# Kernel tuning notes

Hardware: AMD Instinct MI355X
Metric: run time of the kernel (lower is better)

Reference implementation:

```python
import jax, jax.numpy as jnp
import numpy as np

N_NODES = 50000
N_GRAPHS = 256
IN_DIM = 128
HID = 128
N_LAYERS = 3
N_EDGES = 800000


def setup_inputs() -> dict:
    key = jax.random.key(0)
    ks = jax.random.split(key, 16)
    x = jax.random.normal(ks[0], (N_NODES, IN_DIM), dtype=jnp.float32)
    edge_index = jax.random.randint(ks[1], (2, N_EDGES), 0, N_NODES, dtype=jnp.int64)
    batch = jnp.sort(jax.random.randint(ks[2], (N_NODES,), 0, N_GRAPHS, dtype=jnp.int64))
    inp = {"x": x, "edge_index": edge_index, "batch": batch}
    # SAGEConv params per PyG: lin_l (bias) applied to mean-aggregated neighbors,
    # lin_r (no bias) applied to the root node feature.
    dims = [(IN_DIM, HID)] + [(HID, HID)] * (N_LAYERS - 1)
    for i, (din, dout) in enumerate(dims):
        s = 1.0 / np.sqrt(din)
        inp[f"Wl{i}"] = jax.random.uniform(ks[3 + 3 * i], (din, dout), jnp.float32, -s, s)
        inp[f"bl{i}"] = jax.random.uniform(ks[4 + 3 * i], (dout,), jnp.float32, -s, s)
        inp[f"Wr{i}"] = jax.random.uniform(ks[5 + 3 * i], (din, dout), jnp.float32, -s, s)
    return inp


def _sage_conv(x, src, dst, Wl, bl, Wr):
    # mean aggregation of source-node messages into destination nodes
    msg = x[src]                                               # [E, d] gather
    agg = jax.ops.segment_sum(msg, dst, num_segments=N_NODES)  # [N, d] scatter-add
    deg = jax.ops.segment_sum(jnp.ones((src.shape[0], 1), x.dtype), dst,
                              num_segments=N_NODES)
    agg = agg / jnp.maximum(deg, 1.0)
    return agg @ Wl + bl + x @ Wr


def reference(x, edge_index, batch, Wl0, bl0, Wr0, Wl1, bl1, Wr1, Wl2, bl2, Wr2):
    src, dst = edge_index[0], edge_index[1]
    params = [(Wl0, bl0, Wr0), (Wl1, bl1, Wr1), (Wl2, bl2, Wr2)]
    h = x
    for Wl, bl, Wr in params:
        h = jax.nn.relu(_sage_conv(h, src, dst, Wl, bl, Wr))
        # dropout is a no-op in eval mode
    # meanmax readout over graph ids
    cnt = jax.ops.segment_sum(jnp.ones((h.shape[0], 1), h.dtype), batch,
                              num_segments=N_GRAPHS)
    g_mean = jax.ops.segment_sum(h, batch, num_segments=N_GRAPHS) / jnp.maximum(cnt, 1.0)
    g_max = jax.ops.segment_max(h, batch, num_segments=N_GRAPHS)
    g_max = jnp.where(jnp.isfinite(g_max), g_max, 0.0)  # empty graphs -> 0
    return jnp.concatenate([g_mean, g_max], axis=-1)    # [G, 2*HID]
```

## Files before the change

### kernel.cpp

```cpp
#include <hip/hip_runtime.h>
#include <hip/hip_bf16.h>
#include <stdint.h>

#define N_NODES  50000
#define N_GRAPHS 256
#define DIM      128
#define N_EDGES  800000
#define K2       256
#define N_STRIPS (N_NODES / 16)
#define PAD_CAP  64
#define NBUCKET  196
#define NCHUNK   256
#define CHUNK    3125

typedef __attribute__((ext_vector_type(8))) short  short8;
typedef __attribute__((ext_vector_type(4))) float  floatx4;

__device__ __forceinline__ ushort f2bf(float f) {
    union { float f; uint32_t u; } c; c.f = f;
    uint32_t u = c.u;
    return (ushort)((u + 0x7fffu + ((u >> 16) & 1u)) >> 16);
}
__device__ __forceinline__ float bf2f(ushort b) {
    union { uint32_t u; float f; } c; c.u = ((uint32_t)b) << 16;
    return c.f;
}

__global__ __launch_bounds__(256) void k_convert_x(const float* __restrict__ x,
                                                   ushort* __restrict__ xb) {
    int i = blockIdx.x * 256 + threadIdx.x;
    const int n4 = N_NODES * DIM / 4;
    if (i < n4) {
        float4 v = ((const float4*)x)[i];
        uint32_t lo = (uint32_t)f2bf(v.x) | ((uint32_t)f2bf(v.y) << 16);
        uint32_t hi = (uint32_t)f2bf(v.z) | ((uint32_t)f2bf(v.w) << 16);
        ((uint2*)xb)[i] = make_uint2(lo, hi);
    }
}

__global__ __launch_bounds__(256) void k_prep_w_all(const float* __restrict__ Wl0, const float* __restrict__ Wr0,
                                                    const float* __restrict__ Wl1, const float* __restrict__ Wr1,
                                                    const float* __restrict__ Wl2, const float* __restrict__ Wr2,
                                                    ushort* __restrict__ Wt) {
    int i = blockIdx.x * 256 + threadIdx.x;
    if (i < 3 * DIM * K2) {
        int layer = i / (DIM * K2);
        int j = i % (DIM * K2);
        int n = j / K2, k = j % K2;
        const float* Wl = (layer == 0) ? Wl0 : (layer == 1) ? Wl1 : Wl2;
        const float* Wr = (layer == 0) ? Wr0 : (layer == 1) ? Wr1 : Wr2;
        float v = (k < DIM) ? Wl[k * DIM + n] : Wr[(k - DIM) * DIM + n];
        Wt[i] = f2bf(v);
    }
}

__global__ __launch_bounds__(256) void k_hist(const int* __restrict__ dst,
                                              int* __restrict__ counts) {
    __shared__ int hist[NBUCKET];
    int t = threadIdx.x, b = blockIdx.x;
    if (t < NBUCKET) hist[t] = 0;
    __syncthreads();
    const int e0 = b * CHUNK;
    for (int i = t; i < CHUNK; i += 256)
        atomicAdd(&hist[dst[e0 + i] >> 8], 1);
    __syncthreads();
    if (t < NBUCKET) counts[b * NBUCKET + t] = hist[t];
}

__global__ __launch_bounds__(256) void k_scan_col(const int* __restrict__ counts,
                                                  int* __restrict__ off,
                                                  int* __restrict__ total) {
    __shared__ int buf[256];
    int t = threadIdx.x, j = blockIdx.x;
    int v = counts[t * NBUCKET + j];
    buf[t] = v;
    __syncthreads();
    #pragma unroll
    for (int d = 1; d < 256; d <<= 1) {
        int x = (t >= d) ? buf[t - d] : 0;
        __syncthreads();
        buf[t] += x;
        __syncthreads();
    }
    off[t * NBUCKET + j] = buf[t] - v;
    if (t == 255) total[j] = buf[255];
}

__global__ __launch_bounds__(256) void k_scan_total(const int* __restrict__ total,
                                                    int* __restrict__ basep) {
    __shared__ int buf[256];
    int t = threadIdx.x;
    int v = (t < NBUCKET) ? total[t] : 0;
    buf[t] = v;
    __syncthreads();
    #pragma unroll
    for (int d = 1; d < 256; d <<= 1) {
        int x = (t >= d) ? buf[t - d] : 0;
        __syncthreads();
        buf[t] += x;
        __syncthreads();
    }
    if (t < NBUCKET) basep[t] = buf[t] - v;
}

__global__ __launch_bounds__(256) void k_scatter(const int* __restrict__ src,
                                                 const int* __restrict__ dst,
                                                 const int* __restrict__ off,
                                                 const int* __restrict__ basep,
                                                 uint32_t* __restrict__ ebuf) {
    __shared__ int cur[NBUCKET];
    int t = threadIdx.x, b = blockIdx.x;
    if (t < NBUCKET) cur[t] = off[b * NBUCKET + t] + basep[t];
    __syncthreads();
    const int e0 = b * CHUNK;
    for (int i = t; i < CHUNK; i += 256) {
        int d = dst[e0 + i];
        int s = src[e0 + i];
        int p = atomicAdd(&cur[d >> 8], 1);
        ebuf[p] = ((uint32_t)(d & 255) << 16) | (uint32_t)s;
    }
}

__global__ __launch_bounds__(256) void k_build(const uint32_t* __restrict__ ebuf,
                                               const int* __restrict__ total,
                                               const int* __restrict__ basep,
                                               int* __restrict__ padded,
                                               int* __restrict__ cnt) {
    __shared__ int lcnt[256];
    int t = threadIdx.x, j = blockIdx.x;
    lcnt[t] = 0;
    __syncthreads();
    int b0 = basep[j], tot = total[j];
    for (int i = t; i < tot; i += 256) {
        uint32_t v = ebuf[b0 + i];
        int dl = (int)(v >> 16);
        int s  = (int)(v & 0xffffu);
        int p  = atomicAdd(&lcnt[dl], 1);
        if (p < PAD_CAP) padded[((size_t)j * 256 + dl) * PAD_CAP + p] = s;
    }
    __syncthreads();
    int node = j * 256 + t;
    if (node < N_NODES) cnt[node] = lcnt[t];
}

__global__ __launch_bounds__(256) void k_sort_adj(int* __restrict__ padded,
                                                  const int* __restrict__ cnt) {
    int wid  = threadIdx.x >> 6;
    int lane = threadIdx.x & 63;
    int node = blockIdx.x * 4 + wid;
    if (node >= N_NODES) return;
    int deg = cnt[node];
    int m   = deg < PAD_CAP ? deg : PAD_CAP;
    int* lst = padded + (size_t)node * PAD_CAP;
    int v = (lane < m) ? lst[lane] : 0x7fffffff;
    #pragma unroll
    for (int k = 2; k <= 64; k <<= 1) {
        #pragma unroll
        for (int j = k >> 1; j > 0; j >>= 1) {
            int other  = __shfl_xor(v, j, 64);
            bool down  = (lane & k) != 0;
            bool lower = (lane & j) == 0;
            v = (lower ^ down) ? min(v, other) : max(v, other);
        }
    }
    if (lane < m) lst[lane] = v;
}

__global__ __launch_bounds__(256) void k_gbounds(const int* __restrict__ batch,
                                                 int* __restrict__ gstart,
                                                 int* __restrict__ gend) {
    int i = blockIdx.x * 256 + threadIdx.x;
    if (i >= N_NODES) return;
    int g = batch[i];
    if (i == 0) gstart[g] = 0;
    int gn = (i + 1 < N_NODES) ? batch[i + 1] : -1;
    if (gn != g) {
        gend[g] = i + 1;
        if (gn >= 0) gstart[gn] = i + 1;
    }
}

template <bool OUT_F32>
__global__ __launch_bounds__(256) void k_layer(const ushort* __restrict__ h_in,
                                               const int* __restrict__ padded,
                                               const int* __restrict__ cnt,
                                               const ushort* __restrict__ Wt,
                                               const float* __restrict__ bias,
                                               ushort* __restrict__ out_bf,
                                               float* __restrict__ out_f) {
    __shared__ ushort sAgg[16 * DIM];
    int wid  = threadIdx.x >> 6;
    int lane = threadIdx.x & 63;
    int r0   = blockIdx.x * 16;
    const uint32_t* hw = (const uint32_t*)h_in;

    for (int q = 0; q < 4; ++q) {
        int node = r0 + wid * 4 + q;
        int deg = cnt[node];
        int m   = deg < PAD_CAP ? deg : PAD_CAP;
        const int* lst = padded + (size_t)node * PAD_CAP;
        float ax[4] = {0.f, 0.f, 0.f, 0.f};
        float ay[4] = {0.f, 0.f, 0.f, 0.f};
        for (int e = 0; e < m; e += 16) {
            int idx[16];
            uint32_t v[16];
            #pragma unroll
            for (int k = 0; k < 16; ++k) {
                int ek = e + k;
                idx[k] = lst[ek < m ? ek : m - 1];
            }
            #pragma unroll
            for (int k = 0; k < 16; ++k)
                v[k] = hw[(size_t)idx[k] * 64 + lane];
            #pragma unroll
            for (int k = 0; k < 16; ++k) {
                uint32_t w = (e + k < m) ? v[k] : 0u;
                ax[k & 3] += bf2f((ushort)(w & 0xffffu));
                ay[k & 3] += bf2f((ushort)(w >> 16));
            }
        }
        float axs = (ax[0] + ax[1]) + (ax[2] + ax[3]);
        float ays = (ay[0] + ay[1]) + (ay[2] + ay[3]);
        float inv = 1.0f / (float)(deg > 0 ? deg : 1);
        uint32_t o = (uint32_t)f2bf(axs * inv) | ((uint32_t)f2bf(ays * inv) << 16);
        ((uint32_t*)(sAgg + (wid * 4 + q) * DIM))[lane] = o;
    }
    __syncthreads();

    int row  = lane & 15;
    int quad = lane >> 4;
    short8 a[8];
    const ushort* srow = sAgg + row * DIM + quad * 8;
    #pragma unroll
    for (int ks = 0; ks < 4; ++ks) a[ks] = *(const short8*)(srow + ks * 32);
    const ushort* hrow = h_in + (size_t)(r0 + row) * DIM + quad * 8;
    #pragma unroll
    for (int ks = 0; ks < 4; ++ks) a[4 + ks] = *(const short8*)(hrow + ks * 32);

    #pragma unroll
    for (int c = 0; c < 2; ++c) {
        int ct  = wid * 2 + c;
        int col = ct * 16 + row;
        const ushort* wrow = Wt + (size_t)col * K2 + quad * 8;
        floatx4 acc = {0.f, 0.f, 0.f, 0.f};
        #pragma unroll
        for (int ks = 0; ks < 8; ++ks) {
            short8 b = *(const short8*)(wrow + ks * 32);
            acc = __builtin_amdgcn_mfma_f32_16x16x32_bf16(a[ks], b, acc, 0, 0, 0);
        }
        float bv = bias[col];
        #pragma unroll
        for (int r = 0; r < 4; ++r) {
            int m = r0 + quad * 4 + r;
            float v = acc[r] + bv;
            v = v > 0.f ? v : 0.f;
            if (OUT_F32) out_f[(size_t)m * DIM + col] = v;
            else         out_bf[(size_t)m * DIM + col] = f2bf(v);
        }
    }
}

__global__ __launch_bounds__(128) void k_readout(const float* __restrict__ h,
                                                 const int* __restrict__ batch,
                                                 float* __restrict__ out) {
    int d  = threadIdx.x;
    int n0 = blockIdx.x * 128;
    int n1 = min(n0 + 128, N_NODES);
    int cur = -1; float sum = 0.f, mx = 0.f;
    for (int i = n0; i < n1; ++i) {
        int g = batch[i];
        if (g != cur) {
            if (cur >= 0) {
                atomicAdd(&out[cur * 2 * DIM + d], sum);
                atomicMax((int*)&out[cur * 2 * DIM + DIM + d], __float_as_int(mx));
            }
            cur = g; sum = 0.f; mx = 0.f;
        }
        float v = h[(size_t)i * DIM + d];
        sum += v; mx = fmaxf(mx, v);
    }
    if (cur >= 0) {
        atomicAdd(&out[cur * 2 * DIM + d], sum);
        atomicMax((int*)&out[cur * 2 * DIM + DIM + d], __float_as_int(mx));
    }
}

__global__ __launch_bounds__(256) void k_finalize(float* __restrict__ out,
                                                  const int* __restrict__ gstart,
                                                  const int* __restrict__ gend) {
    int i = blockIdx.x * 256 + threadIdx.x;
    if (i < N_GRAPHS * DIM) {
        int g = i / DIM, d = i % DIM;
        int c = gend[g] - gstart[g];
        out[g * 2 * DIM + d] /= (float)(c > 0 ? c : 1);
    }
}

extern "C" void kernel_launch(void* const* d_in, const int* in_sizes, int n_in,
                              void* d_out, int out_size, void* d_ws, size_t ws_size,
                              hipStream_t stream) {
    const float* x     = (const float*)d_in[0];
    const int*   ei    = (const int*)d_in[1];
    const int*   src   = ei;
    const int*   dst   = ei + N_EDGES;
    const int*   batch = (const int*)d_in[2];
    const float* Wl[3] = {(const float*)d_in[3], (const float*)d_in[6], (const float*)d_in[9]};
    const float* bl[3] = {(const float*)d_in[4], (const float*)d_in[7], (const float*)d_in[10]};
    const float* Wr[3] = {(const float*)d_in[5], (const float*)d_in[8], (const float*)d_in[11]};
    float* out = (float*)d_out;

    char* base = (char*)d_ws;
    size_t o = 0;
    auto alloc = [&](size_t b) -> char* {
        char* p = base + o;
        o = (o + b + 255) & ~(size_t)255;
        return p;
    };
    int*     gstart = (int*)alloc((size_t)N_GRAPHS * 4);
    int*     gend   = (int*)alloc((size_t)N_GRAPHS * 4);
    size_t   zero_bytes = o;
    int*     cnt    = (int*)alloc((size_t)N_NODES * 4);
    int*     counts = (int*)alloc((size_t)NCHUNK * NBUCKET * 4);
    int*     offs   = (int*)alloc((size_t)NCHUNK * NBUCKET * 4);
    int*     total  = (int*)alloc((size_t)NBUCKET * 4);
    int*     basep  = (int*)alloc((size_t)NBUCKET * 4);
    uint32_t* ebuf  = (uint32_t*)alloc((size_t)N_EDGES * 4);
    int*     padded = (int*)alloc((size_t)N_NODES * PAD_CAP * 4);
    ushort*  xb     = (ushort*)alloc((size_t)N_NODES * DIM * 2);
    ushort*  ha     = (ushort*)alloc((size_t)N_NODES * DIM * 2);
    ushort*  hb     = (ushort*)alloc((size_t)N_NODES * DIM * 2);
    float*   h3     = (float*)alloc((size_t)N_NODES * DIM * 4);
    ushort*  Wt     = (ushort*)alloc((size_t)3 * DIM * K2 * 2);
    (void)ws_size; (void)n_in; (void)in_sizes;

    hipMemsetAsync(base, 0, zero_bytes, stream);
    hipMemsetAsync(d_out, 0, (size_t)out_size * 4, stream);

    k_convert_x<<<(N_NODES * DIM / 4 + 255) / 256, 256, 0, stream>>>(x, xb);
    k_prep_w_all<<<(3 * DIM * K2 + 255) / 256, 256, 0, stream>>>(
        Wl[0], Wr[0], Wl[1], Wr[1], Wl[2], Wr[2], Wt);

    k_hist<<<NCHUNK, 256, 0, stream>>>(dst, counts);
    k_scan_col<<<NBUCKET, 256, 0, stream>>>(counts, offs, total);
    k_scan_total<<<1, 256, 0, stream>>>(total, basep);
    k_scatter<<<NCHUNK, 256, 0, stream>>>(src, dst, offs, basep, ebuf);
    k_build<<<NBUCKET, 256, 0, stream>>>(ebuf, total, basep, padded, cnt);
    k_sort_adj<<<(N_NODES + 3) / 4, 256, 0, stream>>>(padded, cnt);
    k_gbounds<<<(N_NODES + 255) / 256, 256, 0, stream>>>(batch, gstart, gend);

    k_layer<false><<<N_STRIPS, 256, 0, stream>>>(xb, padded, cnt, Wt,              bl[0], ha, nullptr);
    k_layer<false><<<N_STRIPS, 256, 0, stream>>>(ha, padded, cnt, Wt + DIM * K2,   bl[1], hb, nullptr);
    k_layer<true ><<<N_STRIPS, 256, 0, stream>>>(hb, padded, cnt, Wt + 2 * DIM * K2, bl[2], nullptr, h3);

    k_readout<<<(N_NODES + 127) / 128, 128, 0, stream>>>(h3, batch, out);
    k_finalize<<<(N_GRAPHS * DIM + 255) / 256, 256, 0, stream>>>(out, gstart, gend);
}
```

Measured before the change: 365.1 us.

## Give each node its own wavefront with 16-byte gathers across four edge groups

The layer kernel now launches 1024 threads per block, so each of the 16 wavefronts aggregates one node instead of four. Each wavefront splits into four 16-lane groups that each fetch a full 256-byte neighbor row with uint4 loads, handling four edges at a time. Neighbor indices are broadcast with ds_bpermute, and the partial sums are reduced with cross-lane shuffles. The aggregation buffer in LDS is padded to limit bank conflicts, and only 8 of the 16 waves do the MFMA projection, so the other half sit idle during that phase and the larger blocks may lower occupancy.

Measured after the change: 375.1 us. 1.03x slower.

```diff
diff --git a/kernel.cpp b/kernel.cpp
--- a/kernel.cpp
+++ b/kernel.cpp
@@ -12,6 +12,7 @@
 #define NBUCKET  196
 #define NCHUNK   256
 #define CHUNK    3125
+#define SROW     136
 
 typedef __attribute__((ext_vector_type(8))) short  short8;
 typedef __attribute__((ext_vector_type(4))) float  floatx4;
@@ -24,6 +25,12 @@
 __device__ __forceinline__ float bf2f(ushort b) {
     union { uint32_t u; float f; } c; c.u = ((uint32_t)b) << 16;
     return c.f;
+}
+__device__ __forceinline__ float bflo(uint32_t d) {
+    union { uint32_t u; float f; } c; c.u = d << 16; return c.f;
+}
+__device__ __forceinline__ float bfhi(uint32_t d) {
+    union { uint32_t u; float f; } c; c.u = d & 0xffff0000u; return c.f;
 }
 
 __global__ __launch_bounds__(256) void k_convert_x(const float* __restrict__ x,
@@ -181,81 +188,91 @@
 }
 
 template <bool OUT_F32>
-__global__ __launch_bounds__(256) void k_layer(const ushort* __restrict__ h_in,
-                                               const int* __restrict__ padded,
-                                               const int* __restrict__ cnt,
-                                               const ushort* __restrict__ Wt,
-                                               const float* __restrict__ bias,
-                                               ushort* __restrict__ out_bf,
-                                               float* __restrict__ out_f) {
-    __shared__ ushort sAgg[16 * DIM];
+__global__ __launch_bounds__(1024) void k_layer(const ushort* __restrict__ h_in,
+                                                const int* __restrict__ padded,
+                                                const int* __restrict__ cnt,
+                                                const ushort* __restrict__ Wt,
+                                                const float* __restrict__ bias,
+                                                ushort* __restrict__ out_bf,
+                                                float* __restrict__ out_f) {
+    __shared__ ushort sAgg[16 * SROW];
     int wid  = threadIdx.x >> 6;
     int lane = threadIdx.x & 63;
     int r0   = blockIdx.x * 16;
-    const uint32_t* hw = (const uint32_t*)h_in;
-
-    for (int q = 0; q < 4; ++q) {
-        int node = r0 + wid * 4 + q;
-        int deg = cnt[node];
-        int m   = deg < PAD_CAP ? deg : PAD_CAP;
-        const int* lst = padded + (size_t)node * PAD_CAP;
-        float ax[4] = {0.f, 0.f, 0.f, 0.f};
-        float ay[4] = {0.f, 0.f, 0.f, 0.f};
-        for (int e = 0; e < m; e += 16) {
-            int idx[16];
-            uint32_t v[16];
-            #pragma unroll
-            for (int k = 0; k < 16; ++k) {
-                int ek = e + k;
-                idx[k] = lst[ek < m ? ek : m - 1];
-            }
-            #pragma unroll
-            for (int k = 0; k < 16; ++k)
-                v[k] = hw[(size_t)idx[k] * 64 + lane];
-            #pragma unroll
-            for (int k = 0; k < 16; ++k) {
-                uint32_t w = (e + k < m) ? v[k] : 0u;
-                ax[k & 3] += bf2f((ushort)(w & 0xffffu));
-                ay[k & 3] += bf2f((ushort)(w >> 16));
-            }
-        }
-        float axs = (ax[0] + ax[1]) + (ax[2] + ax[3]);
-        float ays = (ay[0] + ay[1]) + (ay[2] + ay[3]);
+    int node = r0 + wid;
+    int deg  = cnt[node];
+    int m    = deg < PAD_CAP ? deg : PAD_CAP;
+    const int* lst = padded + (size_t)node * PAD_CAP;
+    int vidx = lst[lane];
+    int g    = lane >> 4;
+    int l4   = lane & 15;
+    const char* hbase = (const char*)h_in;
+
+    float acc[8] = {0.f,0.f,0.f,0.f,0.f,0.f,0.f,0.f};
+    for (int base = 0; base < m; base += 16) {
+        uint4 v[4];
+        #pragma unroll
+        for (int s = 0; s < 4; ++s) {
+            int e  = base + s * 4 + g;
+            int ec = e < m ? e : m - 1;
+            int nb = __builtin_amdgcn_ds_bpermute(ec << 2, vidx);
+            v[s] = *(const uint4*)(hbase + ((size_t)(uint32_t)nb << 8) + (l4 << 4));
+        }
+        #pragma unroll
+        for (int s = 0; s < 4; ++s) {
+            int e = base + s * 4 + g;
+            uint32_t d0 = (e < m) ? v[s].x : 0u;
+            uint32_t d1 = (e < m) ? v[s].y : 0u;
+            uint32_t d2 = (e < m) ? v[s].z : 0u;
+            uint32_t d3 = (e < m) ? v[s].w : 0u;
+            acc[0] += bflo(d0); acc[1] += bfhi(d0);
+            acc[2] += bflo(d1); acc[3] += bfhi(d1);
+            acc[4] += bflo(d2); acc[5] += bfhi(d2);
+            acc[6] += bflo(d3); acc[7] += bfhi(d3);
+        }
+    }
+    #pragma unroll
+    for (int j = 0; j < 8; ++j) {
+        acc[j] += __shfl_xor(acc[j], 16, 64);
+        acc[j] += __shfl_xor(acc[j], 32, 64);
+    }
+    if (lane < 16) {
         float inv = 1.0f / (float)(deg > 0 ? deg : 1);
-        uint32_t o = (uint32_t)f2bf(axs * inv) | ((uint32_t)f2bf(ays * inv) << 16);
-        ((uint32_t*)(sAgg + (wid * 4 + q) * DIM))[lane] = o;
-    }
-    __syncthreads();
-
-    int row  = lane & 15;
-    int quad = lane >> 4;
-    short8 a[8];
-    const ushort* srow = sAgg + row * DIM + quad * 8;
-    #pragma unroll
-    for (int ks = 0; ks < 4; ++ks) a[ks] = *(const short8*)(srow + ks * 32);
-    const ushort* hrow = h_in + (size_t)(r0 + row) * DIM + quad * 8;
-    #pragma unroll
-    for (int ks = 0; ks < 4; ++ks) a[4 + ks] = *(const short8*)(hrow + ks * 32);
-
-    #pragma unroll
-    for (int c = 0; c < 2; ++c) {
-        int ct  = wid * 2 + c;
-        int col = ct * 16 + row;
+        uint32_t w0 = (uint32_t)f2bf(acc[0]*inv) | ((uint32_t)f2bf(acc[1]*inv) << 16);
+        uint32_t w1 = (uint32_t)f2bf(acc[2]*inv) | ((uint32_t)f2bf(acc[3]*inv) << 16);
+        uint32_t w2 = (uint32_t)f2bf(acc[4]*inv) | ((uint32_t)f2bf(acc[5]*inv) << 16);
+        uint32_t w3 = (uint32_t)f2bf(acc[6]*inv) | ((uint32_t)f2bf(acc[7]*inv) << 16);
+        *(uint4*)((char*)sAgg + wid * (SROW * 2) + lane * 16) = make_uint4(w0, w1, w2, w3);
+    }
+    __syncthreads();
+
+    if (wid < 8) {
+        int row  = lane & 15;
+        int quad = lane >> 4;
+        short8 a[8];
+        const ushort* srow = sAgg + row * SROW + quad * 8;
+        #pragma unroll
+        for (int ks = 0; ks < 4; ++ks) a[ks] = *(const short8*)(srow + ks * 32);
+        const ushort* hrow = h_in + (size_t)(r0 + row) * DIM + quad * 8;
+        #pragma unroll
+        for (int ks = 0; ks < 4; ++ks) a[4 + ks] = *(const short8*)(hrow + ks * 32);
+
+        int col = wid * 16 + row;
         const ushort* wrow = Wt + (size_t)col * K2 + quad * 8;
-        floatx4 acc = {0.f, 0.f, 0.f, 0.f};
+        floatx4 acc2 = {0.f, 0.f, 0.f, 0.f};
         #pragma unroll
         for (int ks = 0; ks < 8; ++ks) {
             short8 b = *(const short8*)(wrow + ks * 32);
-            acc = __builtin_amdgcn_mfma_f32_16x16x32_bf16(a[ks], b, acc, 0, 0, 0);
+            acc2 = __builtin_amdgcn_mfma_f32_16x16x32_bf16(a[ks], b, acc2, 0, 0, 0);
         }
         float bv = bias[col];
         #pragma unroll
         for (int r = 0; r < 4; ++r) {
-            int m = r0 + quad * 4 + r;
-            float v = acc[r] + bv;
+            int mr = r0 + quad * 4 + r;
+            float v = acc2[r] + bv;
             v = v > 0.f ? v : 0.f;
-            if (OUT_F32) out_f[(size_t)m * DIM + col] = v;
-            else         out_bf[(size_t)m * DIM + col] = f2bf(v);
+            if (OUT_F32) out_f[(size_t)mr * DIM + col] = v;
+            else         out_bf[(size_t)mr * DIM + col] = f2bf(v);
         }
     }
 }
@@ -348,9 +365,9 @@
     k_sort_adj<<<(N_NODES + 3) / 4, 256, 0, stream>>>(padded, cnt);
     k_gbounds<<<(N_NODES + 255) / 256, 256, 0, stream>>>(batch, gstart, gend);
 
-    k_layer<false><<<N_STRIPS, 256, 0, stream>>>(xb, padded, cnt, Wt,              bl[0], ha, nullptr);
-    k_layer<false><<<N_STRIPS, 256, 0, stream>>>(ha, padded, cnt, Wt + DIM * K2,   bl[1], hb, nullptr);
-    k_layer<true ><<<N_STRIPS, 256, 0, stream>>>(hb, padded, cnt, Wt + 2 * DIM * K2, bl[2], nullptr, h3);
+    k_layer<false><<<N_STRIPS, 1024, 0, stream>>>(xb, padded, cnt, Wt,                bl[0], ha, nullptr);
+    k_layer<false><<<N_STRIPS, 1024, 0, stream>>>(ha, padded, cnt, Wt + DIM * K2,     bl[1], hb, nullptr);
+    k_layer<true ><<<N_STRIPS, 1024, 0, stream>>>(hb, padded, cnt, Wt + 2 * DIM * K2, bl[2], nullptr, h3);
 
     k_readout<<<(N_NODES + 127) / 128, 128, 0, stream>>>(h3, batch, out);
     k_finalize<<<(N_GRAPHS * DIM + 255) / 256, 256, 0, stream>>>(out, gstart, gend);
```
